# Performance work log

Hardware: AMD Instinct MI355X
Metric: run time of the kernel (lower is better)

Reference implementation:

```python
import jax, jax.numpy as jnp
import numpy as np

B, T, P = 4096, 128, 2
D_m = D_g = D_p = D_e = 256


def gru_cell(x, h, w_ih, w_hh, b_ih, b_hh):
    # PyTorch GRUCell math
    gi = x @ w_ih.T + b_ih          # [N, 3H]
    gh = h @ w_hh.T + b_hh          # [N, 3H]
    ir, iz, inn = jnp.split(gi, 3, axis=1)
    hr, hz, hn = jnp.split(gh, 3, axis=1)
    r = jax.nn.sigmoid(ir + hr)
    z = jax.nn.sigmoid(iz + hz)
    n = jnp.tanh(inn + r * hn)
    return (1.0 - z) * n + z * h


def _gru_params(key, in_dim, hid):
    k1, k2, k3, k4 = jax.random.split(key, 4)
    s = 1.0 / np.sqrt(hid)
    u = lambda k, shp: jax.random.uniform(k, shp, jnp.float32, -s, s)
    return u(k1, (3 * hid, in_dim)), u(k2, (3 * hid, hid)), u(k3, (3 * hid,)), u(k4, (3 * hid,))


def setup_inputs() -> dict:
    key = jax.random.key(0)
    ks = jax.random.split(key, 10)
    U = jax.random.normal(ks[0], (B, D_m), jnp.float32)
    qm_idx = jax.random.randint(ks[1], (B,), 0, P)
    g_hist = jax.random.normal(ks[2], (T, B, D_g), jnp.float32)
    q0 = jax.random.normal(ks[3], (B, P, D_p), jnp.float32)
    e0 = jax.random.normal(ks[4], (B, D_e), jnp.float32)
    wg = _gru_params(ks[5], D_m + D_p, D_g)
    wp = _gru_params(ks[6], D_m + D_g, D_p)
    we = _gru_params(ks[7], D_p, D_e)
    sa = 1.0 / np.sqrt(D_g)
    attn_w = jax.random.uniform(ks[8], (1, D_g), jnp.float32, -sa, sa)
    return {
        "U": U, "qm_idx": qm_idx, "g_hist": g_hist, "q0": q0, "e0": e0,
        "wg_ih": wg[0], "wg_hh": wg[1], "bg_ih": wg[2], "bg_hh": wg[3],
        "wp_ih": wp[0], "wp_hh": wp[1], "bp_ih": wp[2], "bp_hh": wp[3],
        "we_ih": we[0], "we_hh": we[1], "be_ih": we[2], "be_hh": we[3],
        "attn_w": attn_w,
    }


def reference(U, qm_idx, g_hist, q0, e0,
              wg_ih, wg_hh, bg_ih, bg_hh,
              wp_ih, wp_hh, bp_ih, bp_hh,
              we_ih, we_hh, be_ih, be_hh,
              attn_w):
    b_idx = jnp.arange(U.shape[0])
    qmask = jax.nn.one_hot(qm_idx, P, dtype=U.dtype)             # [B, P]
    # _select_parties: gather the speaking party's state
    q0_sel = q0[b_idx, qm_idx]                                    # [B, D_p]
    # global GRU step (g_hist non-empty -> hidden = g_hist[-1])
    g_ = gru_cell(jnp.concatenate([U, q0_sel], axis=1), g_hist[-1],
                  wg_ih, wg_hh, bg_ih, bg_hh)                     # [B, D_g]
    # SimpleAttention over history: softmax over time of a scalar score
    scale = jnp.einsum('tbd,od->tb', g_hist, attn_w)              # [T, B]
    alpha_t = jax.nn.softmax(scale, axis=0)                       # [T, B]
    c_ = jnp.einsum('tb,tbd->bd', alpha_t, g_hist)                # [B, D_g]
    alpha = alpha_t.T[:, None, :]                                 # [B, 1, T]
    # party GRU applied to every party slot
    U_c = jnp.concatenate([U, c_], axis=1)                        # [B, D_m+D_g]
    U_c_exp = jnp.broadcast_to(U_c[:, None, :], (U.shape[0], P, U_c.shape[1]))
    qs_ = gru_cell(U_c_exp.reshape(-1, D_m + D_g), q0.reshape(-1, D_p),
                   wp_ih, wp_hh, bp_ih, bp_hh).reshape(U.shape[0], P, D_p)
    # listener_state=False: listeners keep q0; speaker slot takes qs_
    qm = qmask[..., None]
    q_ = q0 * (1.0 - qm) + qs_ * qm                               # [B, P, D_p]
    # emotion GRU on the speaking party's updated state
    e_ = gru_cell(q_[b_idx, qm_idx], e0, we_ih, we_hh, be_ih, be_hh)  # [B, D_e]
    return g_, q_, e_, alpha
```

## Files before the change

### kernel.cpp

```cpp
#include <hip/hip_runtime.h>
#include <hip/hip_bf16.h>
#include <cstdint>
#include <cstddef>

#define B_N   4096
#define T_N   128
#define P_N   2
#define D     256
#define NG    768
#define BD    (B_N * D)

typedef __attribute__((ext_vector_type(4))) float f32x4;
typedef __attribute__((ext_vector_type(8))) short bf16x8;
typedef __attribute__((ext_vector_type(8))) unsigned short ushort8;

__device__ __forceinline__ unsigned short f2bf(float f) {
    __hip_bfloat16 h = __float2bfloat16(f);
    return *reinterpret_cast<unsigned short*>(&h);
}

struct CvtJobs {
    const float*     src[9];
    unsigned short*  dst[9];
    int              n[9];
};

__global__ __launch_bounds__(256) void cvt_batch(CvtJobs jobs)
{
    const int j = blockIdx.y;
    const int i = (blockIdx.x * 256 + threadIdx.x) * 8;
    if (i >= jobs.n[j]) return;
    const float4* s = reinterpret_cast<const float4*>(jobs.src[j] + i);
    const float4 v0 = s[0], v1 = s[1];
    ushort8 o = { f2bf(v0.x), f2bf(v0.y), f2bf(v0.z), f2bf(v0.w),
                  f2bf(v1.x), f2bf(v1.y), f2bf(v1.z), f2bf(v1.w) };
    *reinterpret_cast<ushort8*>(jobs.dst[j] + i) = o;
}

__global__ __launch_bounds__(256) void attn_kernel(
    const float* __restrict__ g_hist, const float* __restrict__ attn_w,
    unsigned short* __restrict__ c_bf, float* __restrict__ alpha_out)
{
    const int lane = threadIdx.x & 63;
    const int wid  = threadIdx.x >> 6;
    const int b    = blockIdx.x * 4 + wid;

    const float4 w4 = *reinterpret_cast<const float4*>(attn_w + lane * 4);
    const float* gbase = g_hist + (size_t)b * D + lane * 4;

    float  m = -INFINITY, l = 0.f;
    float4 acc = {0.f, 0.f, 0.f, 0.f};
    float  s0 = 0.f, s1 = 0.f;

    auto step = [&](int t, const float4& g) {
        float dot = g.x * w4.x + g.y * w4.y + g.z * w4.z + g.w * w4.w;
        #pragma unroll
        for (int off = 32; off >= 1; off >>= 1)
            dot += __shfl_xor(dot, off, 64);
        const float mn   = fmaxf(m, dot);
        const float corr = __expf(m - mn);
        const float p    = __expf(dot - mn);
        l = l * corr + p;
        acc.x = fmaf(p, g.x, acc.x * corr);
        acc.y = fmaf(p, g.y, acc.y * corr);
        acc.z = fmaf(p, g.z, acc.z * corr);
        acc.w = fmaf(p, g.w, acc.w * corr);
        m = mn;
        if ((t & 63) == lane) { if (t & 64) s1 = dot; else s0 = dot; }
    };

    for (int t = 0; t < T_N; t += 2) {
        const float4 g0 = *reinterpret_cast<const float4*>(gbase + (size_t)t * BD);
        const float4 g1 = *reinterpret_cast<const float4*>(gbase + (size_t)(t + 1) * BD);
        step(t, g0);
        step(t + 1, g1);
    }

    const float rl = 1.f / l;
    ushort4 cv = { f2bf(acc.x * rl), f2bf(acc.y * rl),
                   f2bf(acc.z * rl), f2bf(acc.w * rl) };
    *reinterpret_cast<ushort4*>(c_bf + (size_t)b * D + lane * 4) = cv;
    alpha_out[(size_t)b * T_N + lane]      = __expf(s0 - m) * rl;
    alpha_out[(size_t)b * T_N + 64 + lane] = __expf(s1 - m) * rl;
}

template<int MODE>
__global__ __launch_bounds__(256) void fused_gru(
    const unsigned short* __restrict__ A0,
    const unsigned short* __restrict__ A1,
    const unsigned short* __restrict__ Wi, int ldwi, int Ki,
    const float* __restrict__ bi,
    const unsigned short* __restrict__ Ah,
    const unsigned short* __restrict__ Wh,
    const float* __restrict__ bh,
    const float* __restrict__ hsrc,
    const int*  __restrict__ qm,
    float* __restrict__ out_f32,
    unsigned short* __restrict__ out_bf)
{
    const int r0 = blockIdx.x * 128;
    const int c0 = blockIdx.y * 32;

    __shared__ unsigned short As[128 * 32];
    __shared__ unsigned short Ws[128 * 32];

    const int tid  = threadIdx.x;
    const int lane = tid & 63;
    const int wid  = tid >> 6;

    const int st_row = lane >> 2;
    const int st_p   = lane & 3;

    f32x4 accI[2][6] = {};
    f32x4 accH[2][6] = {};

    auto kstep = [&](const unsigned short* Apart, int kcolA, int kcolW,
                     const unsigned short* W, int ldw, f32x4 (&acc)[2][6]) {
        #pragma unroll
        for (int c = 0; c < 2; ++c) {
            const int row  = wid * 32 + c * 16 + st_row;
            const int scol = (st_p ^ ((row >> 1) & 3)) * 8;
            __builtin_amdgcn_global_load_lds(
                (const __attribute__((address_space(1))) void*)
                    (Apart + (size_t)(r0 + row) * D + kcolA + scol),
                (__attribute__((address_space(3))) void*)
                    (As + wid * 1024 + c * 512), 16, 0, 0);
            int grp = row >> 5; if (grp == 3) grp = 2;
            const int wrow = grp * 256 + c0 + (row & 31);
            __builtin_amdgcn_global_load_lds(
                (const __attribute__((address_space(1))) void*)
                    (W + (size_t)wrow * ldw + kcolW + scol),
                (__attribute__((address_space(3))) void*)
                    (Ws + wid * 1024 + c * 512), 16, 0, 0);
        }
        __syncthreads();

        const int s  = lane >> 4;
        const int fr = lane & 15;
        bf16x8 a[2], b[6];
        #pragma unroll
        for (int m = 0; m < 2; ++m) {
            const int row = wid * 32 + m * 16 + fr;
            const int ph  = s ^ ((row >> 1) & 3);
            a[m] = *reinterpret_cast<const bf16x8*>(&As[row * 32 + ph * 8]);
        }
        #pragma unroll
        for (int j = 0; j < 6; ++j) {
            const int row = j * 16 + fr;
            const int ph  = s ^ ((row >> 1) & 3);
            b[j] = *reinterpret_cast<const bf16x8*>(&Ws[row * 32 + ph * 8]);
        }
        #pragma unroll
        for (int m = 0; m < 2; ++m)
            #pragma unroll
            for (int j = 0; j < 6; ++j)
                acc[m][j] = __builtin_amdgcn_mfma_f32_16x16x32_bf16(
                    a[m], b[j], acc[m][j], 0, 0, 0);
        __syncthreads();
    };

    for (int kt = 0; kt < Ki; kt += 32) {
        const unsigned short* Ap = (kt < D) ? A0 : A1;
        kstep(Ap, kt & (D - 1), kt, Wi, ldwi, accI);
    }
    for (int kt = 0; kt < D; kt += 32)
        kstep(Ah, kt, kt, Wh, D, accH);

    const int cr = (lane >> 4) * 4;
    const int cc = lane & 15;
    #pragma unroll
    for (int m = 0; m < 2; ++m) {
        #pragma unroll
        for (int jj = 0; jj < 2; ++jj) {
            const int col = c0 + jj * 16 + cc;
            const float bir = bi[col],       bhr = bh[col];
            const float biz = bi[col + 256], bhz = bh[col + 256];
            const float bin = bi[col + 512], bhn = bh[col + 512];
            #pragma unroll
            for (int q = 0; q < 4; ++q) {
                const int row = r0 + wid * 32 + m * 16 + cr + q;
                const float ir  = accI[m][jj][q]     + bir;
                const float hr  = accH[m][jj][q]     + bhr;
                const float iz  = accI[m][jj + 2][q] + biz;
                const float hz  = accH[m][jj + 2][q] + bhz;
                const float in_ = accI[m][jj + 4][q] + bin;
                const float hn  = accH[m][jj + 4][q] + bhn;
                const float rg = 1.f / (1.f + __expf(-(ir + hr)));
                const float zg = 1.f / (1.f + __expf(-(iz + hz)));
                const float ng = tanhf(in_ + rg * hn);
                if (MODE == 1) {
                    const int p = qm[row];
                    const float hv  = hsrc[(size_t)row * 512 + (size_t)p * 256 + col];
                    const float ov  = hsrc[(size_t)row * 512 + (size_t)(1 - p) * 256 + col];
                    const float val = (1.f - zg) * ng + zg * hv;
                    out_f32[(size_t)row * 512 + (size_t)p * 256 + col]       = val;
                    out_f32[(size_t)row * 512 + (size_t)(1 - p) * 256 + col] = ov;
                    out_bf[(size_t)row * 256 + col] = f2bf(val);
                } else {
                    const float hv  = hsrc[(size_t)row * 256 + col];
                    const float val = (1.f - zg) * ng + zg * hv;
                    out_f32[(size_t)row * 256 + col] = val;
                }
            }
        }
    }
}

__global__ __launch_bounds__(256) void gather_q0(
    const float* __restrict__ q0, const int* __restrict__ qm,
    unsigned short* __restrict__ q0_sel_bf)
{
    const int i   = blockIdx.x * 256 + threadIdx.x;
    const int row = i >> 6;
    const int j   = (i & 63) * 4;
    const float4 v = *reinterpret_cast<const float4*>(
        q0 + ((size_t)row * P_N + qm[row]) * D + j);
    ushort4 bv = { f2bf(v.x), f2bf(v.y), f2bf(v.z), f2bf(v.w) };
    *reinterpret_cast<ushort4*>(q0_sel_bf + (size_t)row * D + j) = bv;
}

extern "C" void kernel_launch(void* const* d_in, const int* in_sizes, int n_in,
                              void* d_out, int out_size, void* d_ws, size_t ws_size,
                              hipStream_t stream)
{
    const float* U      = (const float*)d_in[0];
    const int*   qm     = (const int*)  d_in[1];
    const float* g_hist = (const float*)d_in[2];
    const float* q0     = (const float*)d_in[3];
    const float* e0     = (const float*)d_in[4];
    const float* wg_ih  = (const float*)d_in[5];
    const float* wg_hh  = (const float*)d_in[6];
    const float* bg_ih  = (const float*)d_in[7];
    const float* bg_hh  = (const float*)d_in[8];
    const float* wp_ih  = (const float*)d_in[9];
    const float* wp_hh  = (const float*)d_in[10];
    const float* bp_ih  = (const float*)d_in[11];
    const float* bp_hh  = (const float*)d_in[12];
    const float* we_ih  = (const float*)d_in[13];
    const float* we_hh  = (const float*)d_in[14];
    const float* be_ih  = (const float*)d_in[15];
    const float* be_hh  = (const float*)d_in[16];
    const float* attn_w = (const float*)d_in[17];

    float* out   = (float*)d_out;
    float* g_out = out;
    float* q_out = out + 1048576;
    float* e_out = out + 3145728;
    float* a_out = out + 4194304;

    unsigned short* bf = (unsigned short*)d_ws;
    unsigned short* U_bf     = bf;
    unsigned short* e0_bf    = bf + 1048576;
    unsigned short* glast_bf = bf + 2097152;
    unsigned short* q0sel_bf = bf + 3145728;
    unsigned short* c_bf     = bf + 4194304;
    unsigned short* qssel_bf = bf + 5242880;
    unsigned short* wgih_bf  = bf + 6291456;
    unsigned short* wpih_bf  = bf + 6684672;
    unsigned short* wghh_bf  = bf + 7077888;
    unsigned short* wphh_bf  = bf + 7274496;
    unsigned short* weih_bf  = bf + 7471104;
    unsigned short* wehh_bf  = bf + 7667712;

    const float* g_last = g_hist + (size_t)(T_N - 1) * BD;

    const dim3 blk(256);
    const dim3 gridGru(B_N / 128, D / 32);

    CvtJobs jobs;
    jobs.src[0] = wg_ih;  jobs.dst[0] = wgih_bf;  jobs.n[0] = NG * 512;
    jobs.src[1] = wg_hh;  jobs.dst[1] = wghh_bf;  jobs.n[1] = NG * 256;
    jobs.src[2] = wp_ih;  jobs.dst[2] = wpih_bf;  jobs.n[2] = NG * 512;
    jobs.src[3] = wp_hh;  jobs.dst[3] = wphh_bf;  jobs.n[3] = NG * 256;
    jobs.src[4] = we_ih;  jobs.dst[4] = weih_bf;  jobs.n[4] = NG * 256;
    jobs.src[5] = we_hh;  jobs.dst[5] = wehh_bf;  jobs.n[5] = NG * 256;
    jobs.src[6] = U;      jobs.dst[6] = U_bf;     jobs.n[6] = B_N * D;
    jobs.src[7] = e0;     jobs.dst[7] = e0_bf;    jobs.n[7] = B_N * D;
    jobs.src[8] = g_last; jobs.dst[8] = glast_bf; jobs.n[8] = B_N * D;
    cvt_batch<<<dim3(B_N * D / 8 / 256, 9), blk, 0, stream>>>(jobs);

    gather_q0<<<B_N * D / 4 / 256, blk, 0, stream>>>(q0, qm, q0sel_bf);
    attn_kernel<<<B_N / 4, blk, 0, stream>>>(g_hist, attn_w, c_bf, a_out);

    fused_gru<0><<<gridGru, blk, 0, stream>>>(
        U_bf, q0sel_bf, wgih_bf, 512, 512, bg_ih,
        glast_bf, wghh_bf, bg_hh,
        g_last, nullptr, g_out, nullptr);

    fused_gru<1><<<gridGru, blk, 0, stream>>>(
        U_bf, c_bf, wpih_bf, 512, 512, bp_ih,
        q0sel_bf, wphh_bf, bp_hh,
        q0, qm, q_out, qssel_bf);

    fused_gru<0><<<gridGru, blk, 0, stream>>>(
        qssel_bf, nullptr, weih_bf, 256, 256, be_ih,
        e0_bf, wehh_bf, be_hh,
        e0, nullptr, e_out, nullptr);
}
```

Baseline: 184.5 us.

## Overlap attention with independent GRU GEMMs in a single co-scheduled kernel

```diff
diff --git a/kernel.cpp b/kernel.cpp
--- a/kernel.cpp
+++ b/kernel.cpp
@@ -19,153 +19,86 @@
     return *reinterpret_cast<unsigned short*>(&h);
 }
 
-struct CvtJobs {
-    const float*     src[9];
-    unsigned short*  dst[9];
-    int              n[9];
-};
-
-__global__ __launch_bounds__(256) void cvt_batch(CvtJobs jobs)
-{
-    const int j = blockIdx.y;
-    const int i = (blockIdx.x * 256 + threadIdx.x) * 8;
-    if (i >= jobs.n[j]) return;
-    const float4* s = reinterpret_cast<const float4*>(jobs.src[j] + i);
-    const float4 v0 = s[0], v1 = s[1];
-    ushort8 o = { f2bf(v0.x), f2bf(v0.y), f2bf(v0.z), f2bf(v0.w),
-                  f2bf(v1.x), f2bf(v1.y), f2bf(v1.z), f2bf(v1.w) };
-    *reinterpret_cast<ushort8*>(jobs.dst[j] + i) = o;
-}
-
-__global__ __launch_bounds__(256) void attn_kernel(
-    const float* __restrict__ g_hist, const float* __restrict__ attn_w,
-    unsigned short* __restrict__ c_bf, float* __restrict__ alpha_out)
-{
-    const int lane = threadIdx.x & 63;
-    const int wid  = threadIdx.x >> 6;
-    const int b    = blockIdx.x * 4 + wid;
-
-    const float4 w4 = *reinterpret_cast<const float4*>(attn_w + lane * 4);
-    const float* gbase = g_hist + (size_t)b * D + lane * 4;
-
-    float  m = -INFINITY, l = 0.f;
-    float4 acc = {0.f, 0.f, 0.f, 0.f};
-    float  s0 = 0.f, s1 = 0.f;
-
-    auto step = [&](int t, const float4& g) {
-        float dot = g.x * w4.x + g.y * w4.y + g.z * w4.z + g.w * w4.w;
-        #pragma unroll
-        for (int off = 32; off >= 1; off >>= 1)
-            dot += __shfl_xor(dot, off, 64);
-        const float mn   = fmaxf(m, dot);
-        const float corr = __expf(m - mn);
-        const float p    = __expf(dot - mn);
-        l = l * corr + p;
-        acc.x = fmaf(p, g.x, acc.x * corr);
-        acc.y = fmaf(p, g.y, acc.y * corr);
-        acc.z = fmaf(p, g.z, acc.z * corr);
-        acc.w = fmaf(p, g.w, acc.w * corr);
-        m = mn;
-        if ((t & 63) == lane) { if (t & 64) s1 = dot; else s0 = dot; }
-    };
-
-    for (int t = 0; t < T_N; t += 2) {
-        const float4 g0 = *reinterpret_cast<const float4*>(gbase + (size_t)t * BD);
-        const float4 g1 = *reinterpret_cast<const float4*>(gbase + (size_t)(t + 1) * BD);
-        step(t, g0);
-        step(t + 1, g1);
-    }
-
-    const float rl = 1.f / l;
-    ushort4 cv = { f2bf(acc.x * rl), f2bf(acc.y * rl),
-                   f2bf(acc.z * rl), f2bf(acc.w * rl) };
-    *reinterpret_cast<ushort4*>(c_bf + (size_t)b * D + lane * 4) = cv;
-    alpha_out[(size_t)b * T_N + lane]      = __expf(s0 - m) * rl;
-    alpha_out[(size_t)b * T_N + 64 + lane] = __expf(s1 - m) * rl;
-}
-
-template<int MODE>
-__global__ __launch_bounds__(256) void fused_gru(
-    const unsigned short* __restrict__ A0,
-    const unsigned short* __restrict__ A1,
-    const unsigned short* __restrict__ Wi, int ldwi, int Ki,
-    const float* __restrict__ bi,
-    const unsigned short* __restrict__ Ah,
-    const unsigned short* __restrict__ Wh,
-    const float* __restrict__ bh,
-    const float* __restrict__ hsrc,
-    const int*  __restrict__ qm,
-    float* __restrict__ out_f32,
-    unsigned short* __restrict__ out_bf)
-{
-    const int r0 = blockIdx.x * 128;
-    const int c0 = blockIdx.y * 32;
-
-    __shared__ unsigned short As[128 * 32];
-    __shared__ unsigned short Ws[128 * 32];
-
-    const int tid  = threadIdx.x;
-    const int lane = tid & 63;
-    const int wid  = tid >> 6;
-
+__device__ __forceinline__ void kstep(
+    const unsigned short* __restrict__ Apart, int r0, int kcolA,
+    const unsigned short* __restrict__ W, int ldw, int kcolW, int c0,
+    unsigned short* As, unsigned short* Ws, int wid, int lane,
+    f32x4 (&acc)[2][6])
+{
     const int st_row = lane >> 2;
     const int st_p   = lane & 3;
-
-    f32x4 accI[2][6] = {};
-    f32x4 accH[2][6] = {};
-
-    auto kstep = [&](const unsigned short* Apart, int kcolA, int kcolW,
-                     const unsigned short* W, int ldw, f32x4 (&acc)[2][6]) {
-        #pragma unroll
-        for (int c = 0; c < 2; ++c) {
-            const int row  = wid * 32 + c * 16 + st_row;
-            const int scol = (st_p ^ ((row >> 1) & 3)) * 8;
-            __builtin_amdgcn_global_load_lds(
-                (const __attribute__((address_space(1))) void*)
-                    (Apart + (size_t)(r0 + row) * D + kcolA + scol),
-                (__attribute__((address_space(3))) void*)
-                    (As + wid * 1024 + c * 512), 16, 0, 0);
-            int grp = row >> 5; if (grp == 3) grp = 2;
-            const int wrow = grp * 256 + c0 + (row & 31);
-            __builtin_amdgcn_global_load_lds(
-                (const __attribute__((address_space(1))) void*)
-                    (W + (size_t)wrow * ldw + kcolW + scol),
-                (__attribute__((address_space(3))) void*)
-                    (Ws + wid * 1024 + c * 512), 16, 0, 0);
+    #pragma unroll
+    for (int c = 0; c < 2; ++c) {
+        const int row  = wid * 32 + c * 16 + st_row;
+        const int scol = (st_p ^ ((row >> 1) & 3)) * 8;
+        __builtin_amdgcn_global_load_lds(
+            (const __attribute__((address_space(1))) void*)
+                (Apart + (size_t)(r0 + row) * D + kcolA + scol),
+            (__attribute__((address_space(3))) void*)
+                (As + wid * 1024 + c * 512), 16, 0, 0);
+        int grp = row >> 5; if (grp == 3) grp = 2;
+        const int wrow = grp * 256 + c0 + (row & 31);
+        __builtin_amdgcn_global_load_lds(
+            (const __attribute__((address_space(1))) void*)
+                (W + (size_t)wrow * ldw + kcolW + scol),
+            (__attribute__((address_space(3))) void*)
+                (Ws + wid * 1024 + c * 512), 16, 0, 0);
+    }
+    __syncthreads();
+
+    const int s  = lane >> 4;
+    const int fr = lane & 15;
+    bf16x8 a[2], b[6];
+    #pragma unroll
+    for (int m = 0; m < 2; ++m) {
+        const int row = wid * 32 + m * 16 + fr;
+        const int ph  = s ^ ((row >> 1) & 3);
+        a[m] = *reinterpret_cast<const bf16x8*>(&As[row * 32 + ph * 8]);
+    }
+    #pragma unroll
+    for (int j = 0; j < 6; ++j) {
+        const int row = j * 16 + fr;
+        const int ph  = s ^ ((row >> 1) & 3);
+        b[j] = *reinterpret_cast<const bf16x8*>(&Ws[row * 32 + ph * 8]);
+    }
+    #pragma unroll
+    for (int m = 0; m < 2; ++m)
+        #pragma unroll
+        for (int j = 0; j < 6; ++j)
+            acc[m][j] = __builtin_amdgcn_mfma_f32_16x16x32_bf16(
+                a[m], b[j], acc[m][j], 0, 0, 0);
+    __syncthreads();
+}
+
+__device__ __forceinline__ void partial_gemm(
+    const unsigned short* __restrict__ A, const unsigned short* __restrict__ W,
+    int ldw, int r0, int c0, unsigned short* As, unsigned short* Ws,
+    int wid, int lane, float* __restrict__ buf)
+{
+    f32x4 acc[2][6] = {};
+    for (int kt = 0; kt < D; kt += 32)
+        kstep(A, r0, kt, W, ldw, kt, c0, As, Ws, wid, lane, acc);
+    const int cr = (lane >> 4) * 4, cc = lane & 15;
+    #pragma unroll
+    for (int m = 0; m < 2; ++m)
+        #pragma unroll
+        for (int j = 0; j < 6; ++j) {
+            const int col = (j >> 1) * 256 + c0 + (j & 1) * 16 + cc;
+            #pragma unroll
+            for (int q = 0; q < 4; ++q) {
+                const int row = r0 + wid * 32 + m * 16 + cr + q;
+                buf[(size_t)row * NG + col] = acc[m][j][q];
+            }
         }
-        __syncthreads();
-
-        const int s  = lane >> 4;
-        const int fr = lane & 15;
-        bf16x8 a[2], b[6];
-        #pragma unroll
-        for (int m = 0; m < 2; ++m) {
-            const int row = wid * 32 + m * 16 + fr;
-            const int ph  = s ^ ((row >> 1) & 3);
-            a[m] = *reinterpret_cast<const bf16x8*>(&As[row * 32 + ph * 8]);
-        }
-        #pragma unroll
-        for (int j = 0; j < 6; ++j) {
-            const int row = j * 16 + fr;
-            const int ph  = s ^ ((row >> 1) & 3);
-            b[j] = *reinterpret_cast<const bf16x8*>(&Ws[row * 32 + ph * 8]);
-        }
-        #pragma unroll
-        for (int m = 0; m < 2; ++m)
-            #pragma unroll
-            for (int j = 0; j < 6; ++j)
-                acc[m][j] = __builtin_amdgcn_mfma_f32_16x16x32_bf16(
-                    a[m], b[j], acc[m][j], 0, 0, 0);
-        __syncthreads();
-    };
-
-    for (int kt = 0; kt < Ki; kt += 32) {
-        const unsigned short* Ap = (kt < D) ? A0 : A1;
-        kstep(Ap, kt & (D - 1), kt, Wi, ldwi, accI);
-    }
-    for (int kt = 0; kt < D; kt += 32)
-        kstep(Ah, kt, kt, Wh, D, accH);
-
+}
+
+template<int MODE>
+__device__ __forceinline__ void gate_epilogue(
+    f32x4 (&accI)[2][6], f32x4 (&accH)[2][6], int r0, int c0, int wid, int lane,
+    const float* __restrict__ bi, const float* __restrict__ bh,
+    const float* __restrict__ hsrc, const int* __restrict__ qm,
+    float* __restrict__ out_f32, unsigned short* __restrict__ out_bf)
+{
     const int cr = (lane >> 4) * 4;
     const int cc = lane & 15;
     #pragma unroll
@@ -206,6 +139,169 @@
     }
 }
 
+__device__ __forceinline__ void attn_block(
+    int abid, const float* __restrict__ g_hist, const float* __restrict__ attn_w,
+    unsigned short* __restrict__ c_bf, float* __restrict__ alpha_out,
+    int lane, int wid)
+{
+    const int b = abid * 4 + wid;
+
+    const float4 w4 = *reinterpret_cast<const float4*>(attn_w + lane * 4);
+    const float* gbase = g_hist + (size_t)b * D + lane * 4;
+
+    float  m = -INFINITY, l = 0.f;
+    float4 acc = {0.f, 0.f, 0.f, 0.f};
+    float  s0 = 0.f, s1 = 0.f;
+
+    auto step = [&](int t, const float4& g) {
+        float dot = g.x * w4.x + g.y * w4.y + g.z * w4.z + g.w * w4.w;
+        #pragma unroll
+        for (int off = 32; off >= 1; off >>= 1)
+            dot += __shfl_xor(dot, off, 64);
+        const float mn   = fmaxf(m, dot);
+        const float corr = __expf(m - mn);
+        const float p    = __expf(dot - mn);
+        l = l * corr + p;
+        acc.x = fmaf(p, g.x, acc.x * corr);
+        acc.y = fmaf(p, g.y, acc.y * corr);
+        acc.z = fmaf(p, g.z, acc.z * corr);
+        acc.w = fmaf(p, g.w, acc.w * corr);
+        m = mn;
+        if ((t & 63) == lane) { if (t & 64) s1 = dot; else s0 = dot; }
+    };
+
+    for (int t = 0; t < T_N; t += 2) {
+        const float4 g0 = *reinterpret_cast<const float4*>(gbase + (size_t)t * BD);
+        const float4 g1 = *reinterpret_cast<const float4*>(gbase + (size_t)(t + 1) * BD);
+        step(t, g0);
+        step(t + 1, g1);
+    }
+
+    const float rl = 1.f / l;
+    ushort4 cv = { f2bf(acc.x * rl), f2bf(acc.y * rl),
+                   f2bf(acc.z * rl), f2bf(acc.w * rl) };
+    *reinterpret_cast<ushort4*>(c_bf + (size_t)b * D + lane * 4) = cv;
+    alpha_out[(size_t)b * T_N + lane]      = __expf(s0 - m) * rl;
+    alpha_out[(size_t)b * T_N + 64 + lane] = __expf(s1 - m) * rl;
+}
+
+__global__ __launch_bounds__(256) void mega(
+    const float* __restrict__ g_hist, const float* __restrict__ attn_w,
+    unsigned short* __restrict__ c_bf, float* __restrict__ a_out,
+    const unsigned short* __restrict__ U_bf,
+    const unsigned short* __restrict__ q0sel_bf,
+    const unsigned short* __restrict__ glast_bf,
+    const unsigned short* __restrict__ wgih_bf,
+    const unsigned short* __restrict__ wghh_bf,
+    const float* __restrict__ bg_ih, const float* __restrict__ bg_hh,
+    const float* __restrict__ g_last, float* __restrict__ g_out,
+    const unsigned short* __restrict__ wpih_bf,
+    const unsigned short* __restrict__ wphh_bf,
+    float* __restrict__ giP, float* __restrict__ ghP,
+    const unsigned short* __restrict__ e0_bf,
+    const unsigned short* __restrict__ wehh_bf,
+    float* __restrict__ ghE)
+{
+    __shared__ unsigned short As[128 * 32];
+    __shared__ unsigned short Ws[128 * 32];
+
+    const int tid  = threadIdx.x;
+    const int lane = tid & 63;
+    const int wid  = tid >> 6;
+    const int bid  = blockIdx.x;
+    const int grp7 = bid / 7;
+    const int rem  = bid - grp7 * 7;
+
+    if (rem >= 3) {
+        attn_block(grp7 * 4 + (rem - 3), g_hist, attn_w, c_bf, a_out, lane, wid);
+        return;
+    }
+
+    const int gid = grp7 * 3 + rem;
+    const int sub = gid & 255;
+    const int r0  = (sub & 31) * 128;
+    const int c0  = (sub >> 5) * 32;
+
+    if (gid < 256) {
+        f32x4 accI[2][6] = {};
+        f32x4 accH[2][6] = {};
+        for (int kt = 0; kt < 512; kt += 32) {
+            const unsigned short* Ap = (kt < D) ? U_bf : q0sel_bf;
+            kstep(Ap, r0, kt & (D - 1), wgih_bf, 512, kt, c0, As, Ws, wid, lane, accI);
+        }
+        for (int kt = 0; kt < D; kt += 32)
+            kstep(glast_bf, r0, kt, wghh_bf, D, kt, c0, As, Ws, wid, lane, accH);
+        gate_epilogue<0>(accI, accH, r0, c0, wid, lane,
+                         bg_ih, bg_hh, g_last, nullptr, g_out, nullptr);
+    } else if (gid < 512) {
+        partial_gemm(U_bf,     wpih_bf, 512, r0, c0, As, Ws, wid, lane, giP);
+        partial_gemm(q0sel_bf, wphh_bf, D,   r0, c0, As, Ws, wid, lane, ghP);
+    } else {
+        partial_gemm(e0_bf,    wehh_bf, D,   r0, c0, As, Ws, wid, lane, ghE);
+    }
+}
+
+template<int MODE>
+__global__ __launch_bounds__(256) void finish_gru(
+    const unsigned short* __restrict__ A,
+    const unsigned short* __restrict__ Wi, int ldw, int kw0,
+    const float* __restrict__ giPre,
+    const float* __restrict__ ghPre,
+    const float* __restrict__ bi, const float* __restrict__ bh,
+    const float* __restrict__ hsrc, const int* __restrict__ qm,
+    float* __restrict__ out_f32, unsigned short* __restrict__ out_bf)
+{
+    __shared__ unsigned short As[128 * 32];
+    __shared__ unsigned short Ws[128 * 32];
+
+    const int tid  = threadIdx.x;
+    const int lane = tid & 63;
+    const int wid  = tid >> 6;
+    const int r0   = blockIdx.x * 128;
+    const int c0   = blockIdx.y * 32;
+
+    f32x4 accI[2][6] = {};
+    f32x4 accH[2][6];
+
+    const int cr = (lane >> 4) * 4, cc = lane & 15;
+    #pragma unroll
+    for (int m = 0; m < 2; ++m)
+        #pragma unroll
+        for (int j = 0; j < 6; ++j) {
+            const int col = (j >> 1) * 256 + c0 + (j & 1) * 16 + cc;
+            #pragma unroll
+            for (int q = 0; q < 4; ++q) {
+                const size_t row = r0 + wid * 32 + m * 16 + cr + q;
+                if (giPre) accI[m][j][q] = giPre[row * NG + col];
+                accH[m][j][q] = ghPre[row * NG + col];
+            }
+        }
+
+    for (int kt = 0; kt < D; kt += 32)
+        kstep(A, r0, kt, Wi, ldw, kw0 + kt, c0, As, Ws, wid, lane, accI);
+
+    gate_epilogue<MODE>(accI, accH, r0, c0, wid, lane,
+                        bi, bh, hsrc, qm, out_f32, out_bf);
+}
+
+struct CvtJobs {
+    const float*     src[9];
+    unsigned short*  dst[9];
+    int              n[9];
+};
+
+__global__ __launch_bounds__(256) void cvt_batch(CvtJobs jobs)
+{
+    const int j = blockIdx.y;
+    const int i = (blockIdx.x * 256 + threadIdx.x) * 8;
+    if (i >= jobs.n[j]) return;
+    const float4* s = reinterpret_cast<const float4*>(jobs.src[j] + i);
+    const float4 v0 = s[0], v1 = s[1];
+    ushort8 o = { f2bf(v0.x), f2bf(v0.y), f2bf(v0.z), f2bf(v0.w),
+                  f2bf(v1.x), f2bf(v1.y), f2bf(v1.z), f2bf(v1.w) };
+    *reinterpret_cast<ushort8*>(jobs.dst[j] + i) = o;
+}
+
 __global__ __launch_bounds__(256) void gather_q0(
     const float* __restrict__ q0, const int* __restrict__ qm,
     unsigned short* __restrict__ q0_sel_bf)
@@ -261,11 +357,14 @@
     unsigned short* wphh_bf  = bf + 7274496;
     unsigned short* weih_bf  = bf + 7471104;
     unsigned short* wehh_bf  = bf + 7667712;
+    float* fws = (float*)(bf + 7864320);
+    float* giP = fws;
+    float* ghP = fws + 3145728;
+    float* ghE = fws + 6291456;
 
     const float* g_last = g_hist + (size_t)(T_N - 1) * BD;
 
     const dim3 blk(256);
-    const dim3 gridGru(B_N / 128, D / 32);
 
     CvtJobs jobs;
     jobs.src[0] = wg_ih;  jobs.dst[0] = wgih_bf;  jobs.n[0] = NG * 512;
@@ -280,20 +379,18 @@
     cvt_batch<<<dim3(B_N * D / 8 / 256, 9), blk, 0, stream>>>(jobs);
 
     gather_q0<<<B_N * D / 4 / 256, blk, 0, stream>>>(q0, qm, q0sel_bf);
-    attn_kernel<<<B_N / 4, blk, 0, stream>>>(g_hist, attn_w, c_bf, a_out);
-
-    fused_gru<0><<<gridGru, blk, 0, stream>>>(
-        U_bf, q0sel_bf, wgih_bf, 512, 512, bg_ih,
-        glast_bf, wghh_bf, bg_hh,
-        g_last, nullptr, g_out, nullptr);
-
-    fused_gru<1><<<gridGru, blk, 0, stream>>>(
-        U_bf, c_bf, wpih_bf, 512, 512, bp_ih,
-        q0sel_bf, wphh_bf, bp_hh,
-        q0, qm, q_out, qssel_bf);
-
-    fused_gru<0><<<gridGru, blk, 0, stream>>>(
-        qssel_bf, nullptr, weih_bf, 256, 256, be_ih,
-        e0_bf, wehh_bf, be_hh,
-        e0, nullptr, e_out, nullptr);
-}
+
+    mega<<<1792, blk, 0, stream>>>(
+        g_hist, attn_w, c_bf, a_out,
+        U_bf, q0sel_bf, glast_bf, wgih_bf, wghh_bf, bg_ih, bg_hh, g_last, g_out,
+        wpih_bf, wphh_bf, giP, ghP,
+        e0_bf, wehh_bf, ghE);
+
+    finish_gru<1><<<dim3(32, 8), blk, 0, stream>>>(
+        c_bf, wpih_bf, 512, 256, giP, ghP,
+        bp_ih, bp_hh, q0, qm, q_out, qssel_bf);
+
+    finish_gru<0><<<dim3(32, 8), blk, 0, stream>>>(
+        qssel_bf, weih_bf, 256, 0, nullptr, ghE,
+        be_ih, be_hh, e0, nullptr, e_out, nullptr);
+}
```

Measured after the change: 233.6 us. 1.27x slower.

## Triple-buffer LDS staging in fused GRU GEMM with async prefetch

Applied to the files above, without the earlier changes.

```diff
diff --git a/kernel.cpp b/kernel.cpp
--- a/kernel.cpp
+++ b/kernel.cpp
@@ -84,11 +84,11 @@
     alpha_out[(size_t)b * T_N + 64 + lane] = __expf(s1 - m) * rl;
 }
 
-template<int MODE>
+template<int MODE, int NI, int LDWI>
 __global__ __launch_bounds__(256) void fused_gru(
     const unsigned short* __restrict__ A0,
     const unsigned short* __restrict__ A1,
-    const unsigned short* __restrict__ Wi, int ldwi, int Ki,
+    const unsigned short* __restrict__ Wi,
     const float* __restrict__ bi,
     const unsigned short* __restrict__ Ah,
     const unsigned short* __restrict__ Wh,
@@ -98,11 +98,12 @@
     float* __restrict__ out_f32,
     unsigned short* __restrict__ out_bf)
 {
+    constexpr int NT = NI + 8;
+
     const int r0 = blockIdx.x * 128;
     const int c0 = blockIdx.y * 32;
 
-    __shared__ unsigned short As[128 * 32];
-    __shared__ unsigned short Ws[128 * 32];
+    __shared__ unsigned short smem[3 * 8192];
 
     const int tid  = threadIdx.x;
     const int lane = tid & 63;
@@ -114,8 +115,27 @@
     f32x4 accI[2][6] = {};
     f32x4 accH[2][6] = {};
 
-    auto kstep = [&](const unsigned short* Apart, int kcolA, int kcolW,
-                     const unsigned short* W, int ldw, f32x4 (&acc)[2][6]) {
+    auto stage = [&](int step, int buf) {
+        const unsigned short* Apart;
+        const unsigned short* W;
+        int kcolA, kcolW, ldw;
+        if (step < NI) {
+            const int kt = step * 32;
+            Apart = (kt < D) ? A0 : A1;
+            kcolA = kt & (D - 1);
+            kcolW = kt;
+            W     = Wi;
+            ldw   = LDWI;
+        } else {
+            const int kt = (step - NI) * 32;
+            Apart = Ah;
+            kcolA = kt;
+            kcolW = kt;
+            W     = Wh;
+            ldw   = D;
+        }
+        unsigned short* As = smem + buf * 8192;
+        unsigned short* Ws = As + 4096;
         #pragma unroll
         for (int c = 0; c < 2; ++c) {
             const int row  = wid * 32 + c * 16 + st_row;
@@ -133,8 +153,11 @@
                 (__attribute__((address_space(3))) void*)
                     (Ws + wid * 1024 + c * 512), 16, 0, 0);
         }
-        __syncthreads();
-
+    };
+
+    auto compute = [&](int buf, f32x4 (&acc)[2][6]) {
+        const unsigned short* As = smem + buf * 8192;
+        const unsigned short* Ws = As + 4096;
         const int s  = lane >> 4;
         const int fr = lane & 15;
         bf16x8 a[2], b[6];
@@ -156,15 +179,26 @@
             for (int j = 0; j < 6; ++j)
                 acc[m][j] = __builtin_amdgcn_mfma_f32_16x16x32_bf16(
                     a[m], b[j], acc[m][j], 0, 0, 0);
-        __syncthreads();
     };
 
-    for (int kt = 0; kt < Ki; kt += 32) {
-        const unsigned short* Ap = (kt < D) ? A0 : A1;
-        kstep(Ap, kt & (D - 1), kt, Wi, ldwi, accI);
+    stage(0, 0);
+    stage(1, 1);
+
+    int cb = 0, ib = 2;
+    for (int s = 0; s < NT; ++s) {
+        if (s + 2 < NT) stage(s + 2, ib);
+        const int rem = NT - 1 - s;
+        if (rem >= 2)      asm volatile("s_waitcnt vmcnt(8)" ::: "memory");
+        else if (rem == 1) asm volatile("s_waitcnt vmcnt(4)" ::: "memory");
+        else               asm volatile("s_waitcnt vmcnt(0)" ::: "memory");
+        __builtin_amdgcn_sched_barrier(0);
+        __builtin_amdgcn_s_barrier();
+        if (s < NI) compute(cb, accI);
+        else        compute(cb, accH);
+        __builtin_amdgcn_s_barrier();
+        cb = (cb == 2) ? 0 : cb + 1;
+        ib = (ib == 2) ? 0 : ib + 1;
     }
-    for (int kt = 0; kt < D; kt += 32)
-        kstep(Ah, kt, kt, Wh, D, accH);
 
     const int cr = (lane >> 4) * 4;
     const int cc = lane & 15;
@@ -282,18 +316,18 @@
     gather_q0<<<B_N * D / 4 / 256, blk, 0, stream>>>(q0, qm, q0sel_bf);
     attn_kernel<<<B_N / 4, blk, 0, stream>>>(g_hist, attn_w, c_bf, a_out);
 
-    fused_gru<0><<<gridGru, blk, 0, stream>>>(
-        U_bf, q0sel_bf, wgih_bf, 512, 512, bg_ih,
+    fused_gru<0, 16, 512><<<gridGru, blk, 0, stream>>>(
+        U_bf, q0sel_bf, wgih_bf, bg_ih,
         glast_bf, wghh_bf, bg_hh,
         g_last, nullptr, g_out, nullptr);
 
-    fused_gru<1><<<gridGru, blk, 0, stream>>>(
-        U_bf, c_bf, wpih_bf, 512, 512, bp_ih,
+    fused_gru<1, 16, 512><<<gridGru, blk, 0, stream>>>(
+        U_bf, c_bf, wpih_bf, bp_ih,
         q0sel_bf, wphh_bf, bp_hh,
         q0, qm, q_out, qssel_bf);
 
-    fused_gru<0><<<gridGru, blk, 0, stream>>>(
-        qssel_bf, nullptr, weih_bf, 256, 256, be_ih,
+    fused_gru<0, 8, 256><<<gridGru, blk, 0, stream>>>(
+        qssel_bf, nullptr, weih_bf, be_ih,
         e0_bf, wehh_bf, be_hh,
         e0, nullptr, e_out, nullptr);
 }
```

Measured after the change: 166.7 us. -9.7%, faster.
